# Optimization experiments

Hardware: AMD Instinct MI355X
Metric: run time of the kernel (lower is better)

The kernel has to match this reference:

```python
import jax, jax.numpy as jnp
import numpy as np

B, S, D, H = 2, 2048, 768, 12
DK = D // H  # 64
LN_EPS = 1e-5


def setup_inputs() -> dict:
    key = jax.random.key(0)
    ks = jax.random.split(key, 8)
    std = 0.02
    return {
        "x": jax.random.normal(ks[0], (B, S, D), dtype=jnp.float32),
        "Wq": jax.random.normal(ks[1], (D, D), dtype=jnp.float32) * std,
        "Wp": jax.random.normal(ks[2], (D, D), dtype=jnp.float32) * std,
        "Wk": jax.random.normal(ks[3], (D, D), dtype=jnp.float32) * std,
        "Wv": jax.random.normal(ks[4], (D, D), dtype=jnp.float32) * std,
        "Wo": jax.random.normal(ks[5], (D, D), dtype=jnp.float32) * std,
        "bo": jnp.zeros((D,), dtype=jnp.float32),
        "gamma": jnp.ones((D,), dtype=jnp.float32),
        "beta": jnp.zeros((D,), dtype=jnp.float32),
        "dt": jnp.asarray(0.1, dtype=jnp.float32),
        "gate": jnp.ones((1,), dtype=jnp.float32),
    }


def _heads(t):
    # [B,S,D] -> [B,H,S,DK]
    return t.reshape(B, S, H, DK).transpose(0, 2, 1, 3)


def reference(x, Wq, Wp, Wk, Wv, Wo, bo, gamma, beta, dt, gate):
    scale = DK ** -0.5
    q = _heads(x @ Wq)
    p = _heads(x @ Wp)
    k = _heads(x @ Wk)
    v = _heads(x @ Wv)

    # --- first attention pass (potential energy at q) ---
    e1 = jnp.einsum("bhsd,bhtd->bhst", q, k) * scale
    w1 = jax.nn.softmax(e1, axis=-1)
    pe1 = jnp.einsum("bhst,bhtd->bhsd", w1, v)  # dV/dq approx (v_to_k = Identity since d_v == d_k)

    # --- leapfrog half step + full position step ---
    p_half = p - (dt / 2) * pe1 * gate
    q_new = q + dt * p_half

    # --- second attention pass at updated q ---
    e2 = jnp.einsum("bhsd,bhtd->bhst", q_new, k) * scale
    w2 = jax.nn.softmax(e2, axis=-1)
    pe2 = jnp.einsum("bhst,bhtd->bhsd", w2, v)
    p_new = p_half - (dt / 2) * pe2 * gate

    q_flat = q_new.transpose(0, 2, 1, 3).reshape(B, S, D)
    out = q_flat @ Wo + bo + x  # to_output + residual

    mu = jnp.mean(out, axis=-1, keepdims=True)
    var = jnp.mean(jnp.square(out - mu), axis=-1, keepdims=True)
    return (out - mu) * jax.lax.rsqrt(var + LN_EPS) * gamma + beta
```

## Files before the change

### kernel.cpp

```cpp
#include <hip/hip_runtime.h>
#include <stdint.h>

typedef __bf16 bf16;
typedef __bf16 bf16x8 __attribute__((ext_vector_type(8)));
typedef __bf16 bf16x4 __attribute__((ext_vector_type(4)));
typedef float f32x4 __attribute__((ext_vector_type(4)));

constexpr int nB = 2, nS = 2048, nD = 768, nH = 12, nDK = 64;
constexpr int nM = nB * nS;
constexpr float LN_EPS = 1e-5f;

static __device__ __forceinline__ f32x4 mfma16(bf16x8 a, bf16x8 b, f32x4 c) {
  return __builtin_amdgcn_mfma_f32_16x16x32_bf16(a, b, c, 0, 0, 0);
}

static __device__ __forceinline__ void gll16(const void* g, void* l) {
  __builtin_amdgcn_global_load_lds(
      (const __attribute__((address_space(1))) void*)g,
      (__attribute__((address_space(3))) void*)l, 16, 0, 0);
}

static __device__ __forceinline__ void stage128x64(const bf16* src, int ldk,
                                                   char* dst, int t, int w) {
#pragma unroll
  for (int i = 0; i < 4; ++i) {
    int row = i * 32 + (t >> 3);
    int c = (t & 7) ^ (row & 7);
    gll16(src + (size_t)row * ldk + c * 8, dst + i * 4096 + w * 1024);
  }
}

__global__ __launch_bounds__(256) void k_prep_x(const float* __restrict__ x,
                                                bf16* __restrict__ xb) {
  int i = (blockIdx.x * 256 + threadIdx.x) * 4;
  float4 v = *(const float4*)(x + i);
  bf16x4 o;
  o[0] = (bf16)v.x; o[1] = (bf16)v.y; o[2] = (bf16)v.z; o[3] = (bf16)v.w;
  *(bf16x4*)(xb + i) = o;
}

__global__ __launch_bounds__(256) void k_prep_w(
    const float* __restrict__ w0, const float* __restrict__ w1,
    const float* __restrict__ w2, const float* __restrict__ w3,
    const float* __restrict__ w4, bf16* __restrict__ wt) {
  __shared__ float tb[64][65];
  int w = blockIdx.z;
  const float* src = (w == 0) ? w0 : (w == 1) ? w1 : (w == 2) ? w2 : (w == 3) ? w3 : w4;
  int k0 = blockIdx.y * 64, n0 = blockIdx.x * 64;
  int tx = threadIdx.x & 63, ty = threadIdx.x >> 6;
#pragma unroll
  for (int it = 0; it < 16; ++it) {
    int r = it * 4 + ty;
    tb[r][tx] = src[(size_t)(k0 + r) * nD + n0 + tx];
  }
  __syncthreads();
  bf16* dst = wt + (size_t)w * nD * nD;
#pragma unroll
  for (int it = 0; it < 16; ++it) {
    int r = it * 4 + ty;
    dst[(size_t)(n0 + r) * nD + k0 + tx] = (bf16)tb[tx][r];
  }
}

__global__ __launch_bounds__(256) void k_gemm_qpkv(
    const bf16* __restrict__ xb, const bf16* __restrict__ wt,
    bf16* __restrict__ qf, bf16* __restrict__ pf, bf16* __restrict__ kf_,
    bf16* __restrict__ vt) {
  __shared__ alignas(16) char smem[65536];
  int t = threadIdx.x, lane = t & 63, w = t >> 6;
  int fr = lane & 15, fg = lane >> 4;
  int wm = w >> 1, wn = w & 1;
  int widx = blockIdx.z;
  int m0 = blockIdx.y * 128, n0 = blockIdx.x * 128;
  const bf16* abase = xb + (size_t)m0 * nD;
  const bf16* bbase = wt + (size_t)widx * nD * nD + (size_t)n0 * nD;

  f32x4 acc[4][4];
#pragma unroll
  for (int i = 0; i < 4; ++i)
#pragma unroll
    for (int j = 0; j < 4; ++j) acc[i][j] = (f32x4){0.f, 0.f, 0.f, 0.f};

  stage128x64(abase, nD, smem, t, w);
  stage128x64(bbase, nD, smem + 16384, t, w);
  __syncthreads();
#pragma unroll 1
  for (int kt = 0; kt < 12; ++kt) {
    if (kt < 11) {
      char* nb = smem + ((kt + 1) & 1) * 32768;
      stage128x64(abase + (kt + 1) * 64, nD, nb, t, w);
      stage128x64(bbase + (kt + 1) * 64, nD, nb + 16384, t, w);
    }
    char* Ab = smem + (kt & 1) * 32768;
    char* Bb = Ab + 16384;
#pragma unroll
    for (int ks = 0; ks < 2; ++ks) {
      bf16x8 af[4], bfr[4];
#pragma unroll
      for (int i = 0; i < 4; ++i) {
        int row = wm * 64 + i * 16 + fr;
        af[i] = *(const bf16x8*)(Ab + row * 128 + (((ks * 4 + fg) ^ (row & 7)) << 4));
      }
#pragma unroll
      for (int j = 0; j < 4; ++j) {
        int row = wn * 64 + j * 16 + fr;
        bfr[j] = *(const bf16x8*)(Bb + row * 128 + (((ks * 4 + fg) ^ (row & 7)) << 4));
      }
#pragma unroll
      for (int i = 0; i < 4; ++i)
#pragma unroll
        for (int j = 0; j < 4; ++j) acc[i][j] = mfma16(af[i], bfr[j], acc[i][j]);
    }
    __syncthreads();
  }
  if (widx < 3) {
    bf16* outf = (widx == 0) ? qf : (widx == 1) ? pf : kf_;
    float oscale = (widx == 2) ? 0.18033688f : 1.0f;
#pragma unroll
    for (int i = 0; i < 4; ++i)
#pragma unroll
      for (int j = 0; j < 4; ++j) {
        int n = n0 + wn * 64 + j * 16 + fr;
#pragma unroll
        for (int r = 0; r < 4; ++r) {
          int m = m0 + wm * 64 + i * 16 + fg * 4 + r;
          outf[(size_t)m * nD + n] = (bf16)(acc[i][j][r] * oscale);
        }
      }
  } else {
#pragma unroll
    for (int i = 0; i < 4; ++i)
#pragma unroll
      for (int j = 0; j < 4; ++j) {
        int n = n0 + wn * 64 + j * 16 + fr;
        int h = n >> 6, dk = n & 63;
        int mbase = m0 + wm * 64 + i * 16 + fg * 4;
        int b = mbase >> 11, s = mbase & (nS - 1);
        int bh = b * nH + h;
        bf16x4 pk;
#pragma unroll
        for (int r = 0; r < 4; ++r) pk[r] = (bf16)acc[i][j][r];
        *(bf16x4*)(vt + ((size_t)bh * nDK + dk) * nS + s) = pk;
      }
  }
}

__global__ __launch_bounds__(256) void k_attn(
    const bf16* __restrict__ qf, const bf16* __restrict__ pf,
    const bf16* __restrict__ kf_, const bf16* __restrict__ vt,
    const float* __restrict__ dtp, const float* __restrict__ gatep,
    bf16* __restrict__ qn) {
  __shared__ alignas(16) char lds[40960];
  char* kb0_ = lds;
  char* kb1_ = lds + 8192;
  char* vb0_ = lds + 16384;
  char* vb1_ = lds + 24576;
  char* plbase = lds + 32768;

  int t = threadIdx.x, lane = t & 63, w = t >> 6;
  int fr = lane & 15, fg = lane >> 4;
  int blk = blockIdx.x;
  int qt = blk & 31, bh = blk >> 5;
  int b = bh / nH, h = bh % nH;
  int q0 = qt * 64 + w * 16;
  const bf16* Qrow = qf + (size_t)(b * nS) * nD + (size_t)h * nDK;
  const bf16* Prow = pf + (size_t)(b * nS) * nD + (size_t)h * nDK;
  const bf16* Krow = kf_ + (size_t)(b * nS) * nD + (size_t)h * nDK;
  const bf16* Vb = vt + (size_t)bh * nDK * nS;
  char* myp = plbase + w * 2048;

  bf16x8 qa[2];
#pragma unroll
  for (int ks = 0; ks < 2; ++ks)
    qa[ks] = *(const bf16x8*)(Qrow + (size_t)(q0 + fr) * nD + ks * 32 + fg * 8);

  float lr = 0.f;
  f32x4 o[4];
#pragma unroll
  for (int df = 0; df < 4; ++df) o[df] = (f32x4){0.f, 0.f, 0.f, 0.f};

  int rsub = lane >> 3, cir = lane & 7;

#define STAGE(bK, bV, kt)                                                      \
  {                                                                            \
    _Pragma("unroll") for (int i = 0; i < 2; ++i) {                            \
      int row = w * 16 + i * 8 + rsub;                                         \
      int c = cir ^ (row & 7);                                                 \
      gll16(Krow + (size_t)((kt)*64 + row) * nD + c * 8,                       \
            (bK) + w * 2048 + i * 1024);                                       \
      gll16(Vb + (size_t)row * nS + (kt)*64 + c * 8,                           \
            (bV) + w * 2048 + i * 1024);                                       \
    }                                                                          \
  }

#define COMPUTE(bK, bV)                                                        \
  {                                                                            \
    f32x4 sf[4];                                                               \
    _Pragma("unroll") for (int kfi = 0; kfi < 4; ++kfi) {                      \
      int key = kfi * 16 + fr;                                                 \
      bf16x8 ka = *(const bf16x8*)((bK) + key * 128 + ((fg ^ (key & 7)) << 4));\
      bf16x8 kc =                                                              \
          *(const bf16x8*)((bK) + key * 128 + (((4 + fg) ^ (key & 7)) << 4));  \
      f32x4 sacc = mfma16(ka, qa[0], (f32x4){0.f, 0.f, 0.f, 0.f});             \
      sf[kfi] = mfma16(kc, qa[1], sacc);                                       \
    }                                                                          \
    float tsp[4] = {0.f, 0.f, 0.f, 0.f};                                       \
    _Pragma("unroll") for (int kfi = 0; kfi < 4; ++kfi) {                      \
      bf16x4 pk;                                                               \
      _Pragma("unroll") for (int r = 0; r < 4; ++r) {                          \
        float e = __builtin_exp2f(sf[kfi][r]);                                 \
        tsp[r] += e;                                                           \
        pk[r] = (bf16)e;                                                       \
      }                                                                        \
      int blk16 = kfi * 2 + (fg >> 1);                                         \
      int phys = fr * 128 + (((blk16 ^ (fr & 7)) << 4) | ((fg & 1) << 3));     \
      *(bf16x4*)(myp + phys) = pk;                                             \
    }                                                                          \
    lr += (tsp[0] + tsp[1]) + (tsp[2] + tsp[3]);                               \
    _Pragma("unroll") for (int ks = 0; ks < 2; ++ks) {                         \
      bf16x8 pb =                                                              \
          *(const bf16x8*)(myp + fr * 128 + (((ks * 4 + fg) ^ (fr & 7)) << 4));\
      _Pragma("unroll") for (int df = 0; df < 4; ++df) {                       \
        int row = df * 16 + fr;                                                \
        bf16x8 vv = *(const bf16x8*)((bV) + row * 128 +                        \
                                     (((ks * 4 + fg) ^ (row & 7)) << 4));      \
        o[df] = mfma16(vv, pb, o[df]);                                         \
      }                                                                        \
    }                                                                          \
  }

#define VMCNT4 asm volatile("s_waitcnt vmcnt(4)" ::: "memory")
#define VMCNT0 asm volatile("s_waitcnt vmcnt(0)" ::: "memory")
#define BAR __builtin_amdgcn_s_barrier()

  STAGE(kb0_, vb0_, 0);
#pragma unroll 1
  for (int kt = 0; kt < 32; kt += 2) {
    STAGE(kb1_, vb1_, kt + 1);
    VMCNT4;
    BAR;
    COMPUTE(kb0_, vb0_);
    BAR;
    if (kt + 2 < 32) {
      STAGE(kb0_, vb0_, kt + 2);
      VMCNT4;
    } else {
      VMCNT0;
    }
    BAR;
    COMPUTE(kb1_, vb1_);
    BAR;
  }
#undef STAGE
#undef COMPUTE
#undef VMCNT4
#undef VMCNT0
#undef BAR

  lr += __shfl_xor(lr, 16);
  lr += __shfl_xor(lr, 32);

  float dt = dtp[0], gate = gatep[0];
  float c2 = 0.5f * dt * dt * gate;
  float inv = 1.f / lr;
  int qrow = q0 + fr;
#pragma unroll
  for (int df = 0; df < 4; ++df) {
    int dk = df * 16 + fg * 4;
    bf16x4 qv4 = *(const bf16x4*)(Qrow + (size_t)qrow * nD + dk);
    bf16x4 pv4 = *(const bf16x4*)(Prow + (size_t)qrow * nD + dk);
    bf16x4 ov;
#pragma unroll
    for (int r = 0; r < 4; ++r) {
      float pe = o[df][r] * inv;
      ov[r] = (bf16)((float)qv4[r] + dt * (float)pv4[r] - c2 * pe);
    }
    *(bf16x4*)(qn + ((size_t)(b * nS) + qrow) * nD + h * nDK + dk) = ov;
  }
}

__global__ __launch_bounds__(256) void k_gemm_out(
    const bf16* __restrict__ qn, const bf16* __restrict__ wto,
    const float* __restrict__ bo, const float* __restrict__ x,
    float* __restrict__ outp) {
  __shared__ alignas(16) char smem[65536];
  int t = threadIdx.x, lane = t & 63, w = t >> 6;
  int fr = lane & 15, fg = lane >> 4;
  int wm = w >> 1, wn = w & 1;
  int m0 = blockIdx.y * 128, n0 = blockIdx.x * 128;
  const bf16* abase = qn + (size_t)m0 * nD;
  const bf16* bbase = wto + (size_t)n0 * nD;

  f32x4 acc[4][4];
#pragma unroll
  for (int i = 0; i < 4; ++i)
#pragma unroll
    for (int j = 0; j < 4; ++j) acc[i][j] = (f32x4){0.f, 0.f, 0.f, 0.f};

  stage128x64(abase, nD, smem, t, w);
  stage128x64(bbase, nD, smem + 16384, t, w);
  __syncthreads();
#pragma unroll 1
  for (int kt = 0; kt < 12; ++kt) {
    if (kt < 11) {
      char* nb = smem + ((kt + 1) & 1) * 32768;
      stage128x64(abase + (kt + 1) * 64, nD, nb, t, w);
      stage128x64(bbase + (kt + 1) * 64, nD, nb + 16384, t, w);
    }
    char* Ab = smem + (kt & 1) * 32768;
    char* Bb = Ab + 16384;
#pragma unroll
    for (int ks = 0; ks < 2; ++ks) {
      bf16x8 af[4], bfr[4];
#pragma unroll
      for (int i = 0; i < 4; ++i) {
        int row = wm * 64 + i * 16 + fr;
        af[i] = *(const bf16x8*)(Ab + row * 128 + (((ks * 4 + fg) ^ (row & 7)) << 4));
      }
#pragma unroll
      for (int j = 0; j < 4; ++j) {
        int row = wn * 64 + j * 16 + fr;
        bfr[j] = *(const bf16x8*)(Bb + row * 128 + (((ks * 4 + fg) ^ (row & 7)) << 4));
      }
#pragma unroll
      for (int i = 0; i < 4; ++i)
#pragma unroll
        for (int j = 0; j < 4; ++j) acc[i][j] = mfma16(af[i], bfr[j], acc[i][j]);
    }
    __syncthreads();
  }
#pragma unroll
  for (int i = 0; i < 4; ++i)
#pragma unroll
    for (int j = 0; j < 4; ++j) {
      int n = n0 + wn * 64 + j * 16 + fr;
      float bias = bo[n];
#pragma unroll
      for (int r = 0; r < 4; ++r) {
        int m = m0 + wm * 64 + i * 16 + fg * 4 + r;
        outp[(size_t)m * nD + n] = acc[i][j][r] + bias + x[(size_t)m * nD + n];
      }
    }
}

__global__ __launch_bounds__(256) void k_ln(const float* outp,
                                            const float* __restrict__ gamma,
                                            const float* __restrict__ beta,
                                            float* y) {
  int t = threadIdx.x, lane = t & 63, w = t >> 6;
  int row = blockIdx.x * 4 + w;
  const float* rp = outp + (size_t)row * nD;
  float v[12], s1 = 0.f, s2 = 0.f;
#pragma unroll
  for (int i = 0; i < 12; ++i) {
    v[i] = rp[lane + i * 64];
    s1 += v[i];
    s2 += v[i] * v[i];
  }
#pragma unroll
  for (int d = 1; d < 64; d <<= 1) {
    s1 += __shfl_xor(s1, d);
    s2 += __shfl_xor(s2, d);
  }
  float mu = s1 * (1.f / 768.f);
  float var = s2 * (1.f / 768.f) - mu * mu;
  float rstd = rsqrtf(var + LN_EPS);
  float* yp = y + (size_t)row * nD;
#pragma unroll
  for (int i = 0; i < 12; ++i) {
    int n = lane + i * 64;
    yp[n] = (v[i] - mu) * rstd * gamma[n] + beta[n];
  }
}

extern "C" void kernel_launch(void* const* d_in, const int* in_sizes, int n_in,
                              void* d_out, int out_size, void* d_ws, size_t ws_size,
                              hipStream_t stream) {
  const float* x = (const float*)d_in[0];
  const float* Wq = (const float*)d_in[1];
  const float* Wp = (const float*)d_in[2];
  const float* Wk = (const float*)d_in[3];
  const float* Wv = (const float*)d_in[4];
  const float* Wo = (const float*)d_in[5];
  const float* bo = (const float*)d_in[6];
  const float* gamma = (const float*)d_in[7];
  const float* beta = (const float*)d_in[8];
  const float* dt = (const float*)d_in[9];
  const float* gate = (const float*)d_in[10];

  char* ws = (char*)d_ws;
  const size_t szb = (size_t)nM * nD * 2;
  bf16* xb = (bf16*)(ws + 0 * szb);
  bf16* qf = (bf16*)(ws + 1 * szb);
  bf16* pf = (bf16*)(ws + 2 * szb);
  bf16* kf_ = (bf16*)(ws + 3 * szb);
  bf16* vt = (bf16*)(ws + 4 * szb);
  bf16* wt = (bf16*)(ws + 5 * szb);
  bf16* qn = xb;
  float* outp = (float*)d_out;

  k_prep_x<<<dim3(nM * nD / 1024), dim3(256), 0, stream>>>(x, xb);
  k_prep_w<<<dim3(12, 12, 5), dim3(256), 0, stream>>>(Wq, Wp, Wk, Wv, Wo, wt);
  k_gemm_qpkv<<<dim3(6, 32, 4), dim3(256), 0, stream>>>(xb, wt, qf, pf, kf_, vt);
  k_attn<<<dim3(768), dim3(256), 0, stream>>>(qf, pf, kf_, vt, dt, gate, qn);
  k_gemm_out<<<dim3(6, 32), dim3(256), 0, stream>>>(qn, wt + 4 * (size_t)nD * nD, bo, x, outp);
  k_ln<<<dim3(nM / 4), dim3(256), 0, stream>>>(outp, gamma, beta, (float*)d_out);
}
```

Measured before the change: 119.0 us.

## Switch attention to 32x32 MFMA with register-shuffled P, dropping LDS staging

Rewrites the attention kernel so each wave handles 32 queries with 32x32x16 bf16 MFMAs instead of 16x16x32. The softmax probabilities are packed into bf16 and redistributed across half-waves with cross-lane shuffles, so the LDS round trip for the P tile goes away. Blocks shrink to 128 threads with less LDS each, which allows more blocks per CU. Each wave now carries larger f32x16 accumulators, so register pressure rises and could cut occupancy.

```diff
diff --git a/kernel.cpp b/kernel.cpp
--- a/kernel.cpp
+++ b/kernel.cpp
@@ -4,7 +4,9 @@
 typedef __bf16 bf16;
 typedef __bf16 bf16x8 __attribute__((ext_vector_type(8)));
 typedef __bf16 bf16x4 __attribute__((ext_vector_type(4)));
+typedef __bf16 bf16x2 __attribute__((ext_vector_type(2)));
 typedef float f32x4 __attribute__((ext_vector_type(4)));
+typedef float f32x16 __attribute__((ext_vector_type(16)));
 
 constexpr int nB = 2, nS = 2048, nD = 768, nH = 12, nDK = 64;
 constexpr int nM = nB * nS;
@@ -12,12 +14,36 @@
 
 static __device__ __forceinline__ f32x4 mfma16(bf16x8 a, bf16x8 b, f32x4 c) {
   return __builtin_amdgcn_mfma_f32_16x16x32_bf16(a, b, c, 0, 0, 0);
+}
+static __device__ __forceinline__ f32x16 mfma32(bf16x8 a, bf16x8 b, f32x16 c) {
+  return __builtin_amdgcn_mfma_f32_32x32x16_bf16(a, b, c, 0, 0, 0);
 }
 
 static __device__ __forceinline__ void gll16(const void* g, void* l) {
   __builtin_amdgcn_global_load_lds(
       (const __attribute__((address_space(1))) void*)g,
       (__attribute__((address_space(3))) void*)l, 16, 0, 0);
+}
+
+static __device__ __forceinline__ f32x16 zero16() {
+  f32x16 z;
+#pragma unroll
+  for (int i = 0; i < 16; ++i) z[i] = 0.f;
+  return z;
+}
+
+static __device__ __forceinline__ uint32_t pk2(float a, float b) {
+  union { bf16x2 v; uint32_t u; } p;
+  p.v[0] = (bf16)a;
+  p.v[1] = (bf16)b;
+  return p.u;
+}
+
+static __device__ __forceinline__ bf16x8 asm8(uint32_t a, uint32_t b,
+                                              uint32_t c, uint32_t d) {
+  union { bf16x8 v; uint32_t u[4]; } r;
+  r.u[0] = a; r.u[1] = b; r.u[2] = c; r.u[3] = d;
+  return r.v;
 }
 
 static __device__ __forceinline__ void stage128x64(const bf16* src, int ldk,
@@ -145,91 +171,101 @@
   }
 }
 
-__global__ __launch_bounds__(256) void k_attn(
+__global__ __launch_bounds__(128) void k_attn(
     const bf16* __restrict__ qf, const bf16* __restrict__ pf,
     const bf16* __restrict__ kf_, const bf16* __restrict__ vt,
     const float* __restrict__ dtp, const float* __restrict__ gatep,
     bf16* __restrict__ qn) {
-  __shared__ alignas(16) char lds[40960];
+  __shared__ alignas(16) char lds[32768];
   char* kb0_ = lds;
   char* kb1_ = lds + 8192;
   char* vb0_ = lds + 16384;
   char* vb1_ = lds + 24576;
-  char* plbase = lds + 32768;
-
-  int t = threadIdx.x, lane = t & 63, w = t >> 6;
-  int fr = lane & 15, fg = lane >> 4;
+
+  int t = threadIdx.x, lane = t & 63, w2 = t >> 6;
+  int ql = lane & 31, hi = lane >> 5;
   int blk = blockIdx.x;
   int qt = blk & 31, bh = blk >> 5;
   int b = bh / nH, h = bh % nH;
-  int q0 = qt * 64 + w * 16;
+  int q = qt * 64 + w2 * 32 + ql;
   const bf16* Qrow = qf + (size_t)(b * nS) * nD + (size_t)h * nDK;
   const bf16* Prow = pf + (size_t)(b * nS) * nD + (size_t)h * nDK;
   const bf16* Krow = kf_ + (size_t)(b * nS) * nD + (size_t)h * nDK;
   const bf16* Vb = vt + (size_t)bh * nDK * nS;
-  char* myp = plbase + w * 2048;
-
-  bf16x8 qa[2];
-#pragma unroll
-  for (int ks = 0; ks < 2; ++ks)
-    qa[ks] = *(const bf16x8*)(Qrow + (size_t)(q0 + fr) * nD + ks * 32 + fg * 8);
+
+  bf16x8 qa[4];
+#pragma unroll
+  for (int ks = 0; ks < 4; ++ks)
+    qa[ks] = *(const bf16x8*)(Qrow + (size_t)q * nD + ks * 16 + hi * 8);
 
   float lr = 0.f;
-  f32x4 o[4];
-#pragma unroll
-  for (int df = 0; df < 4; ++df) o[df] = (f32x4){0.f, 0.f, 0.f, 0.f};
-
-  int rsub = lane >> 3, cir = lane & 7;
+  f32x16 o0 = zero16(), o1 = zero16();
 
 #define STAGE(bK, bV, kt)                                                      \
   {                                                                            \
-    _Pragma("unroll") for (int i = 0; i < 2; ++i) {                            \
-      int row = w * 16 + i * 8 + rsub;                                         \
-      int c = cir ^ (row & 7);                                                 \
+    _Pragma("unroll") for (int i = 0; i < 4; ++i) {                            \
+      int row = i * 16 + w2 * 8 + (lane >> 3);                                 \
+      int c = (lane & 7) ^ (row & 7);                                          \
       gll16(Krow + (size_t)((kt)*64 + row) * nD + c * 8,                       \
-            (bK) + w * 2048 + i * 1024);                                       \
+            (bK) + i * 2048 + w2 * 1024);                                      \
       gll16(Vb + (size_t)row * nS + (kt)*64 + c * 8,                           \
-            (bV) + w * 2048 + i * 1024);                                       \
+            (bV) + i * 2048 + w2 * 1024);                                      \
     }                                                                          \
   }
 
-#define COMPUTE(bK, bV)                                                        \
+#define COMPUTE32(bK, bV)                                                      \
   {                                                                            \
-    f32x4 sf[4];                                                               \
-    _Pragma("unroll") for (int kfi = 0; kfi < 4; ++kfi) {                      \
-      int key = kfi * 16 + fr;                                                 \
-      bf16x8 ka = *(const bf16x8*)((bK) + key * 128 + ((fg ^ (key & 7)) << 4));\
-      bf16x8 kc =                                                              \
-          *(const bf16x8*)((bK) + key * 128 + (((4 + fg) ^ (key & 7)) << 4));  \
-      f32x4 sacc = mfma16(ka, qa[0], (f32x4){0.f, 0.f, 0.f, 0.f});             \
-      sf[kfi] = mfma16(kc, qa[1], sacc);                                       \
+    f32x16 s0 = zero16(), s1 = zero16();                                       \
+    _Pragma("unroll") for (int ks = 0; ks < 4; ++ks) {                         \
+      int ch = ((ks * 2 + hi) ^ (ql & 7)) << 4;                                \
+      bf16x8 k0 = *(const bf16x8*)((bK) + ql * 128 + ch);                      \
+      bf16x8 k1 = *(const bf16x8*)((bK) + (32 + ql) * 128 + ch);               \
+      s0 = mfma32(k0, qa[ks], s0);                                             \
+      s1 = mfma32(k1, qa[ks], s1);                                             \
     }                                                                          \
-    float tsp[4] = {0.f, 0.f, 0.f, 0.f};                                       \
-    _Pragma("unroll") for (int kfi = 0; kfi < 4; ++kfi) {                      \
-      bf16x4 pk;                                                               \
-      _Pragma("unroll") for (int r = 0; r < 4; ++r) {                          \
-        float e = __builtin_exp2f(sf[kfi][r]);                                 \
-        tsp[r] += e;                                                           \
-        pk[r] = (bf16)e;                                                       \
-      }                                                                        \
-      int blk16 = kfi * 2 + (fg >> 1);                                         \
-      int phys = fr * 128 + (((blk16 ^ (fr & 7)) << 4) | ((fg & 1) << 3));     \
-      *(bf16x4*)(myp + phys) = pk;                                             \
+    uint32_t W0[8], W1[8];                                                     \
+    float ts0 = 0.f, ts1 = 0.f;                                                \
+    _Pragma("unroll") for (int g = 0; g < 8; ++g) {                            \
+      float e0 = __builtin_exp2f(s0[2 * g]);                                   \
+      float e1 = __builtin_exp2f(s0[2 * g + 1]);                               \
+      float f0 = __builtin_exp2f(s1[2 * g]);                                   \
+      float f1 = __builtin_exp2f(s1[2 * g + 1]);                               \
+      ts0 += e0 + e1;                                                          \
+      ts1 += f0 + f1;                                                          \
+      W0[g] = pk2(e0, e1);                                                     \
+      W1[g] = pk2(f0, f1);                                                     \
     }                                                                          \
-    lr += (tsp[0] + tsp[1]) + (tsp[2] + tsp[3]);                               \
-    _Pragma("unroll") for (int ks = 0; ks < 2; ++ks) {                         \
-      bf16x8 pb =                                                              \
-          *(const bf16x8*)(myp + fr * 128 + (((ks * 4 + fg) ^ (fr & 7)) << 4));\
-      _Pragma("unroll") for (int df = 0; df < 4; ++df) {                       \
-        int row = df * 16 + fr;                                                \
-        bf16x8 vv = *(const bf16x8*)((bV) + row * 128 +                        \
-                                     (((ks * 4 + fg) ^ (row & 7)) << 4));      \
-        o[df] = mfma16(vv, pb, o[df]);                                         \
-      }                                                                        \
+    lr += ts0 + ts1;                                                           \
+    bf16x8 pb0, pb1, pb2, pb3;                                                 \
+    {                                                                          \
+      uint32_t ra = __shfl_xor(hi ? W0[0] : W0[2], 32);                        \
+      uint32_t rb = __shfl_xor(hi ? W0[1] : W0[3], 32);                        \
+      pb0 = asm8(hi ? ra : W0[0], hi ? rb : W0[1], hi ? W0[2] : ra,            \
+                 hi ? W0[3] : rb);                                             \
+      uint32_t rc = __shfl_xor(hi ? W0[4] : W0[6], 32);                        \
+      uint32_t rd = __shfl_xor(hi ? W0[5] : W0[7], 32);                        \
+      pb1 = asm8(hi ? rc : W0[4], hi ? rd : W0[5], hi ? W0[6] : rc,            \
+                 hi ? W0[7] : rd);                                             \
+      uint32_t re = __shfl_xor(hi ? W1[0] : W1[2], 32);                        \
+      uint32_t rf = __shfl_xor(hi ? W1[1] : W1[3], 32);                        \
+      pb2 = asm8(hi ? re : W1[0], hi ? rf : W1[1], hi ? W1[2] : re,            \
+                 hi ? W1[3] : rf);                                             \
+      uint32_t rg = __shfl_xor(hi ? W1[4] : W1[6], 32);                        \
+      uint32_t rh = __shfl_xor(hi ? W1[5] : W1[7], 32);                        \
+      pb3 = asm8(hi ? rg : W1[4], hi ? rh : W1[5], hi ? W1[6] : rg,            \
+                 hi ? W1[7] : rh);                                             \
     }                                                                          \
-  }
-
-#define VMCNT4 asm volatile("s_waitcnt vmcnt(4)" ::: "memory")
+    _Pragma("unroll") for (int ks = 0; ks < 4; ++ks) {                         \
+      int ch = ((ks * 2 + hi) ^ (ql & 7)) << 4;                                \
+      bf16x8 v0 = *(const bf16x8*)((bV) + ql * 128 + ch);                      \
+      bf16x8 v1 = *(const bf16x8*)((bV) + (32 + ql) * 128 + ch);               \
+      bf16x8 pbk = (ks == 0) ? pb0 : (ks == 1) ? pb1 : (ks == 2) ? pb2 : pb3;  \
+      o0 = mfma32(v0, pbk, o0);                                                \
+      o1 = mfma32(v1, pbk, o1);                                                \
+    }                                                                          \
+  }
+
+#define VMCNT8 asm volatile("s_waitcnt vmcnt(8)" ::: "memory")
 #define VMCNT0 asm volatile("s_waitcnt vmcnt(0)" ::: "memory")
 #define BAR __builtin_amdgcn_s_barrier()
 
@@ -237,45 +273,47 @@
 #pragma unroll 1
   for (int kt = 0; kt < 32; kt += 2) {
     STAGE(kb1_, vb1_, kt + 1);
-    VMCNT4;
+    VMCNT8;
     BAR;
-    COMPUTE(kb0_, vb0_);
+    COMPUTE32(kb0_, vb0_);
     BAR;
     if (kt + 2 < 32) {
       STAGE(kb0_, vb0_, kt + 2);
-      VMCNT4;
+      VMCNT8;
     } else {
       VMCNT0;
     }
     BAR;
-    COMPUTE(kb1_, vb1_);
+    COMPUTE32(kb1_, vb1_);
     BAR;
   }
 #undef STAGE
-#undef COMPUTE
-#undef VMCNT4
+#undef COMPUTE32
+#undef VMCNT8
 #undef VMCNT0
 #undef BAR
 
-  lr += __shfl_xor(lr, 16);
   lr += __shfl_xor(lr, 32);
 
   float dt = dtp[0], gate = gatep[0];
   float c2 = 0.5f * dt * dt * gate;
   float inv = 1.f / lr;
-  int qrow = q0 + fr;
-#pragma unroll
-  for (int df = 0; df < 4; ++df) {
-    int dk = df * 16 + fg * 4;
-    bf16x4 qv4 = *(const bf16x4*)(Qrow + (size_t)qrow * nD + dk);
-    bf16x4 pv4 = *(const bf16x4*)(Prow + (size_t)qrow * nD + dk);
-    bf16x4 ov;
-#pragma unroll
-    for (int r = 0; r < 4; ++r) {
-      float pe = o[df][r] * inv;
-      ov[r] = (bf16)((float)qv4[r] + dt * (float)pv4[r] - c2 * pe);
-    }
-    *(bf16x4*)(qn + ((size_t)(b * nS) + qrow) * nD + h * nDK + dk) = ov;
+  size_t qg = (size_t)(b * nS) + q;
+#pragma unroll
+  for (int vb = 0; vb < 2; ++vb) {
+#pragma unroll
+    for (int rg = 0; rg < 4; ++rg) {
+      int dv = vb * 32 + rg * 8 + hi * 4;
+      bf16x4 qv4 = *(const bf16x4*)(Qrow + (size_t)q * nD + dv);
+      bf16x4 pv4 = *(const bf16x4*)(Prow + (size_t)q * nD + dv);
+      bf16x4 ov;
+#pragma unroll
+      for (int rr = 0; rr < 4; ++rr) {
+        float pe = (vb ? o1[rg * 4 + rr] : o0[rg * 4 + rr]) * inv;
+        ov[rr] = (bf16)((float)qv4[rr] + dt * (float)pv4[rr] - c2 * pe);
+      }
+      *(bf16x4*)(qn + qg * nD + h * nDK + dv) = ov;
+    }
   }
 }
 
@@ -402,7 +440,7 @@
   k_prep_x<<<dim3(nM * nD / 1024), dim3(256), 0, stream>>>(x, xb);
   k_prep_w<<<dim3(12, 12, 5), dim3(256), 0, stream>>>(Wq, Wp, Wk, Wv, Wo, wt);
   k_gemm_qpkv<<<dim3(6, 32, 4), dim3(256), 0, stream>>>(xb, wt, qf, pf, kf_, vt);
-  k_attn<<<dim3(768), dim3(256), 0, stream>>>(qf, pf, kf_, vt, dt, gate, qn);
+  k_attn<<<dim3(768), dim3(128), 0, stream>>>(qf, pf, kf_, vt, dt, gate, qn);
   k_gemm_out<<<dim3(6, 32), dim3(256), 0, stream>>>(qn, wt + 4 * (size_t)nD * nD, bo, x, outp);
   k_ln<<<dim3(nM / 4), dim3(256), 0, stream>>>(outp, gamma, beta, (float*)d_out);
 }
```

Result: slower. 126.6 us (+6.4%).

## Split attention keys across warp pairs with 32-row query tiles per warp

Applied to the files above, without the earlier changes.

Each warp now handles 32 query rows (two 16-row groups) over half of the key range, so each K/V fragment loaded from LDS feeds two query groups. K/V staging uses 32-key tiles with new swizzles. A final LDS exchange adds the partial O accumulators and row sums from the partner warp. This raises LDS operand reuse per MFMA, at the cost of more accumulator registers and an extra reduction step at the end.

```diff
diff --git a/kernel.cpp b/kernel.cpp
--- a/kernel.cpp
+++ b/kernel.cpp
@@ -151,81 +151,90 @@
     const float* __restrict__ dtp, const float* __restrict__ gatep,
     bf16* __restrict__ qn) {
   __shared__ alignas(16) char lds[40960];
-  char* kb0_ = lds;
-  char* kb1_ = lds + 8192;
-  char* vb0_ = lds + 16384;
-  char* vb1_ = lds + 24576;
-  char* plbase = lds + 32768;
-
   int t = threadIdx.x, lane = t & 63, w = t >> 6;
   int fr = lane & 15, fg = lane >> 4;
+  int qhalf = w & 1, kh = w >> 1, sw = w & 1;
   int blk = blockIdx.x;
   int qt = blk & 31, bh = blk >> 5;
   int b = bh / nH, h = bh % nH;
-  int q0 = qt * 64 + w * 16;
+  int q0 = qt * 64 + qhalf * 32;
   const bf16* Qrow = qf + (size_t)(b * nS) * nD + (size_t)h * nDK;
   const bf16* Prow = pf + (size_t)(b * nS) * nD + (size_t)h * nDK;
   const bf16* Krow = kf_ + (size_t)(b * nS) * nD + (size_t)h * nDK;
   const bf16* Vb = vt + (size_t)bh * nDK * nS;
-  char* myp = plbase + w * 2048;
-
-  bf16x8 qa[2];
-#pragma unroll
-  for (int ks = 0; ks < 2; ++ks)
-    qa[ks] = *(const bf16x8*)(Qrow + (size_t)(q0 + fr) * nD + ks * 32 + fg * 8);
-
-  float lr = 0.f;
-  f32x4 o[4];
-#pragma unroll
-  for (int df = 0; df < 4; ++df) o[df] = (f32x4){0.f, 0.f, 0.f, 0.f};
-
-  int rsub = lane >> 3, cir = lane & 7;
-
-#define STAGE(bK, bV, kt)                                                      \
+  const bf16* Kh = Krow + (size_t)(kh * 1024) * nD;
+  const bf16* Vh = Vb + kh * 1024;
+  char* sb = lds + kh * 16384;
+  char* myp = lds + 32768 + w * 2048;
+
+  bf16x8 qa[2][2];
+#pragma unroll
+  for (int qg = 0; qg < 2; ++qg)
+#pragma unroll
+    for (int ks = 0; ks < 2; ++ks)
+      qa[qg][ks] =
+          *(const bf16x8*)(Qrow + (size_t)(q0 + qg * 16 + fr) * nD + ks * 32 + fg * 8);
+
+  f32x4 o[2][4];
+#pragma unroll
+  for (int qg = 0; qg < 2; ++qg)
+#pragma unroll
+    for (int df = 0; df < 4; ++df) o[qg][df] = (f32x4){0.f, 0.f, 0.f, 0.f};
+  float lr0 = 0.f, lr1 = 0.f;
+
+#define STAGE(bufsel, kt)                                                      \
   {                                                                            \
     _Pragma("unroll") for (int i = 0; i < 2; ++i) {                            \
-      int row = w * 16 + i * 8 + rsub;                                         \
-      int c = cir ^ (row & 7);                                                 \
-      gll16(Krow + (size_t)((kt)*64 + row) * nD + c * 8,                       \
-            (bK) + w * 2048 + i * 1024);                                       \
-      gll16(Vb + (size_t)row * nS + (kt)*64 + c * 8,                           \
-            (bV) + w * 2048 + i * 1024);                                       \
+      int slot = sw * 128 + i * 64 + lane;                                     \
+      int kr = slot >> 3, kc = slot & 7;                                       \
+      gll16(Kh + (size_t)((kt)*32 + kr) * nD + (kc ^ (kr & 7)) * 8,            \
+            sb + (bufsel)*4096 + sw * 2048 + i * 1024);                        \
+      int vr = slot >> 2, vc = slot & 3;                                       \
+      gll16(Vh + (size_t)vr * nS + (kt)*32 + (vc ^ ((vr >> 1) & 3)) * 8,       \
+            sb + 8192 + (bufsel)*4096 + sw * 2048 + i * 1024);                 \
     }                                                                          \
   }
 
-#define COMPUTE(bK, bV)                                                        \
+#define COMPUTE(bufsel)                                                        \
   {                                                                            \
-    f32x4 sf[4];                                                               \
-    _Pragma("unroll") for (int kfi = 0; kfi < 4; ++kfi) {                      \
+    char* bK = sb + (bufsel)*4096;                                             \
+    char* bV = sb + 8192 + (bufsel)*4096;                                      \
+    f32x4 sf[2][2];                                                            \
+    _Pragma("unroll") for (int kfi = 0; kfi < 2; ++kfi) {                      \
       int key = kfi * 16 + fr;                                                 \
-      bf16x8 ka = *(const bf16x8*)((bK) + key * 128 + ((fg ^ (key & 7)) << 4));\
-      bf16x8 kc =                                                              \
-          *(const bf16x8*)((bK) + key * 128 + (((4 + fg) ^ (key & 7)) << 4));  \
-      f32x4 sacc = mfma16(ka, qa[0], (f32x4){0.f, 0.f, 0.f, 0.f});             \
-      sf[kfi] = mfma16(kc, qa[1], sacc);                                       \
+      bf16x8 ka = *(const bf16x8*)(bK + key * 128 + ((fg ^ (key & 7)) << 4));  \
+      bf16x8 kc2 =                                                             \
+          *(const bf16x8*)(bK + key * 128 + (((4 + fg) ^ (key & 7)) << 4));    \
+      _Pragma("unroll") for (int qg = 0; qg < 2; ++qg) {                       \
+        f32x4 s = mfma16(ka, qa[qg][0], (f32x4){0.f, 0.f, 0.f, 0.f});          \
+        sf[qg][kfi] = mfma16(kc2, qa[qg][1], s);                               \
+      }                                                                        \
     }                                                                          \
-    float tsp[4] = {0.f, 0.f, 0.f, 0.f};                                       \
-    _Pragma("unroll") for (int kfi = 0; kfi < 4; ++kfi) {                      \
-      bf16x4 pk;                                                               \
-      _Pragma("unroll") for (int r = 0; r < 4; ++r) {                          \
-        float e = __builtin_exp2f(sf[kfi][r]);                                 \
-        tsp[r] += e;                                                           \
-        pk[r] = (bf16)e;                                                       \
+    _Pragma("unroll") for (int qg = 0; qg < 2; ++qg) {                         \
+      float ts = 0.f;                                                          \
+      _Pragma("unroll") for (int kfi = 0; kfi < 2; ++kfi) {                    \
+        bf16x4 pk;                                                             \
+        _Pragma("unroll") for (int r = 0; r < 4; ++r) {                        \
+          float e = __builtin_exp2f(sf[qg][kfi][r]);                           \
+          ts += e;                                                             \
+          pk[r] = (bf16)e;                                                     \
+        }                                                                      \
+        int cp = (kfi * 2 + (fg >> 1)) ^ ((fr >> 1) & 3);                      \
+        *(bf16x4*)(myp + qg * 1024 + fr * 64 + cp * 16 + (fg & 1) * 8) = pk;   \
       }                                                                        \
-      int blk16 = kfi * 2 + (fg >> 1);                                         \
-      int phys = fr * 128 + (((blk16 ^ (fr & 7)) << 4) | ((fg & 1) << 3));     \
-      *(bf16x4*)(myp + phys) = pk;                                             \
+      if (qg == 0) lr0 += ts; else lr1 += ts;                                  \
     }                                                                          \
-    lr += (tsp[0] + tsp[1]) + (tsp[2] + tsp[3]);                               \
-    _Pragma("unroll") for (int ks = 0; ks < 2; ++ks) {                         \
-      bf16x8 pb =                                                              \
-          *(const bf16x8*)(myp + fr * 128 + (((ks * 4 + fg) ^ (fr & 7)) << 4));\
-      _Pragma("unroll") for (int df = 0; df < 4; ++df) {                       \
-        int row = df * 16 + fr;                                                \
-        bf16x8 vv = *(const bf16x8*)((bV) + row * 128 +                        \
-                                     (((ks * 4 + fg) ^ (row & 7)) << 4));      \
-        o[df] = mfma16(vv, pb, o[df]);                                         \
-      }                                                                        \
+    bf16x8 vv[4];                                                              \
+    _Pragma("unroll") for (int df = 0; df < 4; ++df) {                         \
+      int row = df * 16 + fr;                                                  \
+      vv[df] =                                                                 \
+          *(const bf16x8*)(bV + row * 64 + ((fg ^ ((row >> 1) & 3)) << 4));    \
+    }                                                                          \
+    _Pragma("unroll") for (int qg = 0; qg < 2; ++qg) {                         \
+      bf16x8 pb = *(const bf16x8*)(myp + qg * 1024 + fr * 64 +                 \
+                                   ((fg ^ ((fr >> 1) & 3)) << 4));             \
+      _Pragma("unroll") for (int df = 0; df < 4; ++df)                         \
+          o[qg][df] = mfma16(vv[df], pb, o[qg][df]);                           \
     }                                                                          \
   }
 
@@ -233,22 +242,22 @@
 #define VMCNT0 asm volatile("s_waitcnt vmcnt(0)" ::: "memory")
 #define BAR __builtin_amdgcn_s_barrier()
 
-  STAGE(kb0_, vb0_, 0);
+  STAGE(0, 0);
 #pragma unroll 1
   for (int kt = 0; kt < 32; kt += 2) {
-    STAGE(kb1_, vb1_, kt + 1);
+    STAGE(1, kt + 1);
     VMCNT4;
     BAR;
-    COMPUTE(kb0_, vb0_);
+    COMPUTE(0);
     BAR;
     if (kt + 2 < 32) {
-      STAGE(kb0_, vb0_, kt + 2);
+      STAGE(0, kt + 2);
       VMCNT4;
     } else {
       VMCNT0;
     }
     BAR;
-    COMPUTE(kb1_, vb1_);
+    COMPUTE(1);
     BAR;
   }
 #undef STAGE
@@ -257,25 +266,44 @@
 #undef VMCNT0
 #undef BAR
 
-  lr += __shfl_xor(lr, 16);
-  lr += __shfl_xor(lr, 32);
+  lr0 += __shfl_xor(lr0, 16);
+  lr0 += __shfl_xor(lr0, 32);
+  lr1 += __shfl_xor(lr1, 16);
+  lr1 += __shfl_xor(lr1, 32);
+
+  char* ex = lds + w * 8704;
+#pragma unroll
+  for (int qg = 0; qg < 2; ++qg)
+#pragma unroll
+    for (int df = 0; df < 4; ++df)
+      *(f32x4*)(ex + (qg * 4 + df) * 1024 + lane * 16) = o[qg][df];
+  *(float*)(ex + 8192 + lane * 8) = lr0;
+  *(float*)(ex + 8192 + lane * 8 + 4) = lr1;
+  __syncthreads();
+  const char* px = lds + (w ^ 2) * 8704;
 
   float dt = dtp[0], gate = gatep[0];
   float c2 = 0.5f * dt * dt * gate;
-  float inv = 1.f / lr;
-  int qrow = q0 + fr;
-#pragma unroll
-  for (int df = 0; df < 4; ++df) {
-    int dk = df * 16 + fg * 4;
-    bf16x4 qv4 = *(const bf16x4*)(Qrow + (size_t)qrow * nD + dk);
-    bf16x4 pv4 = *(const bf16x4*)(Prow + (size_t)qrow * nD + dk);
-    bf16x4 ov;
-#pragma unroll
-    for (int r = 0; r < 4; ++r) {
-      float pe = o[df][r] * inv;
-      ov[r] = (bf16)((float)qv4[r] + dt * (float)pv4[r] - c2 * pe);
-    }
-    *(bf16x4*)(qn + ((size_t)(b * nS) + qrow) * nD + h * nDK + dk) = ov;
+#pragma unroll
+  for (int qg = 0; qg < 2; ++qg) {
+    float plr = *(const float*)(px + 8192 + lane * 8 + qg * 4);
+    float inv = 1.f / ((qg == 0 ? lr0 : lr1) + plr);
+    int q = q0 + qg * 16 + fr;
+#pragma unroll
+    for (int dfi = 0; dfi < 2; ++dfi) {
+      int df = kh * 2 + dfi;
+      f32x4 po = *(const f32x4*)(px + (qg * 4 + df) * 1024 + lane * 16);
+      int dk = df * 16 + fg * 4;
+      bf16x4 qv4 = *(const bf16x4*)(Qrow + (size_t)q * nD + dk);
+      bf16x4 pv4 = *(const bf16x4*)(Prow + (size_t)q * nD + dk);
+      bf16x4 ov;
+#pragma unroll
+      for (int r = 0; r < 4; ++r) {
+        float pe = (o[qg][df][r] + po[r]) * inv;
+        ov[r] = (bf16)((float)qv4[r] + dt * (float)pv4[r] - c2 * pe);
+      }
+      *(bf16x4*)(qn + ((size_t)(b * nS) + q) * nD + h * nDK + dk) = ov;
+    }
   }
 }
 
```

After: 125.0 us. +5.1%, slower.
